# Optimization experiments

Hardware: AMD Instinct MI355X
Metric: run time of the kernel (lower is better)

Reference implementation:

```python
import jax, jax.numpy as jnp
import numpy as np

HIDDEN = 2048
NUM_HEADS = 16
HEAD_DIM = HIDDEN // NUM_HEADS  # 128
ROPE_THETA = 10000.0
T = 4096


def _rope(x, positions):
    # x: [T, H, D]; neox-style rotary (rotate halves), matching vLLM get_rope default
    half = HEAD_DIM // 2
    inv_freq = 1.0 / (ROPE_THETA ** (jnp.arange(0, half, dtype=jnp.float32) / half))
    freqs = positions.astype(jnp.float32)[:, None] * inv_freq[None, :]  # [T, half]
    cos = jnp.cos(freqs)[:, None, :]  # [T, 1, half]
    sin = jnp.sin(freqs)[:, None, :]
    x1, x2 = x[..., :half], x[..., half:]
    return jnp.concatenate([x1 * cos - x2 * sin, x2 * cos + x1 * sin], axis=-1)


def setup_inputs() -> dict:
    key = jax.random.key(0)
    k1, k2, k3 = jax.random.split(key, 3)
    return {
        "hidden_states": jax.random.normal(k1, (T, HIDDEN), dtype=jnp.float32),
        "positions": jnp.arange(T, dtype=jnp.int32),
        "w_qkv": jax.random.normal(k2, (HIDDEN, 3 * HIDDEN), dtype=jnp.float32) * (HIDDEN ** -0.5),
        "w_o": jax.random.normal(k3, (HIDDEN, HIDDEN), dtype=jnp.float32) * (HIDDEN ** -0.5),
    }


def reference(hidden_states, positions, w_qkv, w_o):
    qkv = hidden_states @ w_qkv  # [T, 3H]
    q, k, v = jnp.split(qkv, 3, axis=-1)
    q = q.reshape(T, NUM_HEADS, HEAD_DIM)
    k = k.reshape(T, NUM_HEADS, HEAD_DIM)
    v = v.reshape(T, NUM_HEADS, HEAD_DIM)
    q = _rope(q, positions)
    k = _rope(k, positions)
    scale = HEAD_DIM ** -0.5
    # causal SDPA over flattened single sequence
    scores = jnp.einsum("qhd,khd->hqk", q, k) * scale  # [H, T, T]
    causal = jnp.tril(jnp.ones((T, T), dtype=bool))
    scores = jnp.where(causal[None, :, :], scores, jnp.finfo(scores.dtype).min)
    probs = jax.nn.softmax(scores, axis=-1)
    attn = jnp.einsum("hqk,khd->qhd", probs, v).reshape(T, HIDDEN)
    return attn @ w_o
```

## Files before the change

kernel.cpp:

```cpp
#include <hip/hip_runtime.h>
#include <hip/hip_bf16.h>
#include <cstdint>
#include <cstddef>

#define T_SEQ 4096
#define HID   2048
#define NH    16
#define HD    128
#define QKVN  6144
#define KVB   32
#define CHT   16
#define CPH   144
#define SCL2  0.12753224f

typedef unsigned short u16;
typedef unsigned int u32;
typedef __bf16 bf16x8 __attribute__((ext_vector_type(8)));
typedef __bf16 bf16x4 __attribute__((ext_vector_type(4)));
typedef float  f32x4  __attribute__((ext_vector_type(4)));

typedef const __attribute__((address_space(1))) void* gas_ptr;
typedef __attribute__((address_space(3))) void* las_ptr;

__device__ __forceinline__ void async16(const void* g, void* l) {
  __builtin_amdgcn_global_load_lds((gas_ptr)g, (las_ptr)l, 16, 0, 0);
}

__device__ __forceinline__ u16 f2bf(float f) {
  unsigned int u = __float_as_uint(f);
  u += 0x7fffu + ((u >> 16) & 1u);
  return (u16)(u >> 16);
}

__device__ __forceinline__ float bf2f(u16 x) {
  return __uint_as_float((unsigned)x << 16);
}

__global__ void cast_f32_bf16(const float* __restrict__ in, u16* __restrict__ out, int n) {
  int i = (blockIdx.x * blockDim.x + threadIdx.x) * 4;
  if (i >= n) return;
  float4 v = *(const float4*)&in[i];
  uint2 o;
  o.x = (unsigned)f2bf(v.x) | ((unsigned)f2bf(v.y) << 16);
  o.y = (unsigned)f2bf(v.z) | ((unsigned)f2bf(v.w) << 16);
  *(uint2*)&out[i] = o;
}

__global__ void transpose_cast(const float* __restrict__ in, u16* __restrict__ out,
                               int R, int C) {
  __shared__ float tile[64][65];
  int c0 = blockIdx.x * 64, r0 = blockIdx.y * 64;
  int tid = threadIdx.x;
#pragma unroll
  for (int i = 0; i < 16; ++i) {
    int e = i * 256 + tid;
    int rr = e >> 6, cc = e & 63;
    tile[rr][cc] = in[(size_t)(r0 + rr) * C + c0 + cc];
  }
  __syncthreads();
#pragma unroll
  for (int i = 0; i < 16; ++i) {
    int e = i * 256 + tid;
    int oc = e >> 6, orr = e & 63;
    out[(size_t)(c0 + oc) * R + r0 + orr] = f2bf(tile[orr][oc]);
  }
}

__global__ void cs_init(const int* __restrict__ pos, float2* __restrict__ cs) {
  int idx = blockIdx.x * 256 + threadIdx.x;
  int t = idx >> 6, dt = idx & 63;
  float inv = exp2f((float)dt * -0.20762050594046932f);
  float f = (float)pos[t] * inv;
  float s, c;
  __sincosf(f, &s, &c);
  cs[idx] = make_float2(c, s);
}

template <int MODE, typename OUT>
__global__ __launch_bounds__(256)
void gemm_bf16_bt(const u16* __restrict__ A, const u16* __restrict__ BT,
                  OUT* __restrict__ C, u16* __restrict__ Qh, u16* __restrict__ Kh,
                  const float2* __restrict__ cs, int M, int N, int K) {
  __shared__ u16 As[2][128 * 32];
  __shared__ u16 Bs[2][128 * 32];
  int tid = threadIdx.x;
  int row0 = blockIdx.y * 128, col0 = blockIdx.x * 128;
  int wv = tid >> 6, lane = tid & 63, lr = lane & 15, lq = lane >> 4;
  int wm = wv * 32;
  f32x4 acc[2][8] = {};

  auto stage = [&](int buf, int ks) {
#pragma unroll
    for (int k = 0; k < 2; ++k) {
      int c = k * 256 + tid;
      int row = c >> 2, col = c & 3;
      int key = (row >> 1) & 3;
      async16(&A[(size_t)(row0 + row) * K + ks + (col ^ key) * 8], &As[buf][c * 8]);
      async16(&BT[(size_t)(col0 + row) * K + ks + (col ^ key) * 8], &Bs[buf][c * 8]);
    }
  };

  stage(0, 0);
  __syncthreads();
  int nk = K >> 5;
  for (int t = 0; t < nk; ++t) {
    int cur = t & 1;
    if (t + 1 < nk) stage(cur ^ 1, (t + 1) * 32);

    const char* AsB = (const char*)&As[cur][0];
    const char* BsB = (const char*)&Bs[cur][0];
    bf16x8 a[2], b[8];
#pragma unroll
    for (int mi = 0; mi < 2; ++mi) {
      int row = wm + mi * 16 + lr;
      a[mi] = *(const bf16x8*)(AsB + row * 64 + ((lq ^ ((row >> 1) & 3)) << 4));
    }
#pragma unroll
    for (int ni = 0; ni < 8; ++ni) {
      int row = ni * 16 + lr;
      b[ni] = *(const bf16x8*)(BsB + row * 64 + ((lq ^ ((row >> 1) & 3)) << 4));
    }
#pragma unroll
    for (int mi = 0; mi < 2; ++mi)
#pragma unroll
      for (int ni = 0; ni < 8; ++ni)
        acc[mi][ni] = __builtin_amdgcn_mfma_f32_16x16x32_bf16(a[mi], b[ni], acc[mi][ni], 0, 0, 0);
    __syncthreads();
  }

  if constexpr (MODE == 1) {
    int sec = col0 >> 11;
    int hh = (col0 & (HID - 1)) >> 7;
    if (sec < 2) {
      u16* dst = (sec == 0) ? Qh : Kh;
      float scl = (sec == 0) ? SCL2 : 1.0f;
#pragma unroll
      for (int mi = 0; mi < 2; ++mi)
#pragma unroll
        for (int r = 0; r < 4; ++r) {
          int t = row0 + wm + mi * 16 + lq * 4 + r;
#pragma unroll
          for (int nj = 0; nj < 4; ++nj) {
            float2 csv = cs[t * 64 + nj * 16 + lr];
            float v1 = acc[mi][nj][r], v2 = acc[mi][nj + 4][r];
            float o1 = (v1 * csv.x - v2 * csv.y) * scl;
            float o2 = (v2 * csv.x + v1 * csv.y) * scl;
            size_t ob = ((size_t)hh * T_SEQ + t) * HD + nj * 16 + lr;
            dst[ob] = f2bf(o1);
            dst[ob + 64] = f2bf(o2);
          }
        }
    } else {
#pragma unroll
      for (int mi = 0; mi < 2; ++mi)
#pragma unroll
        for (int ni = 0; ni < 8; ++ni)
#pragma unroll
          for (int r = 0; r < 4; ++r)
            C[(size_t)(row0 + wm + mi * 16 + lq * 4 + r) * N + col0 + ni * 16 + lr] =
                (OUT)f2bf(acc[mi][ni][r]);
    }
  } else {
#pragma unroll
    for (int mi = 0; mi < 2; ++mi)
#pragma unroll
      for (int ni = 0; ni < 8; ++ni)
#pragma unroll
        for (int r = 0; r < 4; ++r)
          C[(size_t)(row0 + wm + mi * 16 + lq * 4 + r) * N + col0 + ni * 16 + lr] =
              (OUT)acc[mi][ni][r];
  }
}

__global__ void vtrans(const u16* __restrict__ qkv, u16* __restrict__ Vt) {
  __shared__ u16 tile[64][136];
  int t0 = blockIdx.x * 64;
  int h = blockIdx.y;
  int tid = threadIdx.x;
#pragma unroll
  for (int i = 0; i < 32; ++i) {
    int e = i * 256 + tid;
    int tt = e >> 7, d = e & 127;
    tile[tt][d] = qkv[(size_t)(t0 + tt) * QKVN + 2 * HID + h * HD + d];
  }
  __syncthreads();
#pragma unroll
  for (int i = 0; i < 32; ++i) {
    int e = i * 256 + tid;
    int d = e >> 6, tt = e & 63;
    Vt[((size_t)h * HD + d) * T_SEQ + t0 + tt] = tile[tt][d];
  }
}

__global__ __launch_bounds__(256)
void attn_fwd(const u16* __restrict__ Qh, const u16* __restrict__ Kh,
              const u16* __restrict__ Vt, u16* __restrict__ Opart,
              float2* __restrict__ ml, u16* __restrict__ attn) {
  __shared__ u16 Ks[2][32 * 128];
  __shared__ u16 Vs[2][128 * 32];
  __shared__ u16 Ps[4][32 * 32];

  int tid = threadIdx.x;
  int wv = tid >> 6, lane = tid & 63, lr = lane & 15, lq = lane >> 4;
  char* PsB = (char*)&Ps[wv][0];

  int id = blockIdx.x;
  int h = id / CPH;
  int w = (CPH - 1) - (id - h * CPH);
  int slot = h * CPH + w;
  int bq = 0, acc = 0;
  for (;;) {
    int ch = (bq + 4) >> 2;
    if (w < acc + ch) break;
    acc += ch;
    ++bq;
  }
  int c = w - acc;
  int nt = 4 * bq + 4;
  int j0 = c * CHT, j1 = min(j0 + CHT, nt);
  int q0 = bq * 128, wrow0 = q0 + wv * 32;

  bf16x8 qf[2][4];
#pragma unroll
  for (int qi = 0; qi < 2; ++qi)
#pragma unroll
    for (int kd = 0; kd < 4; ++kd)
      qf[qi][kd] = *(const bf16x8*)
          &Qh[((size_t)h * T_SEQ + wrow0 + qi * 16 + lr) * HD + kd * 32 + lq * 8];

  f32x4 acc_ot[8][2] = {};
  float m_run[2] = {-1e30f, -1e30f};
  float l_run[2] = {0.0f, 0.0f};

  auto stage = [&](int buf, int jb) {
#pragma unroll
    for (int k = 0; k < 2; ++k) {
      int cc = k * 256 + tid;
      int row = cc >> 4;
      int sc = (cc ^ (row & 7)) & 15;
      async16(&Kh[((size_t)h * T_SEQ + jb + row) * HD + sc * 8], &Ks[buf][cc * 8]);
    }
#pragma unroll
    for (int k = 0; k < 2; ++k) {
      int cc = k * 256 + tid;
      int row = cc >> 2, col = cc & 3;
      int key = (row >> 1) & 3;
      async16(&Vt[((size_t)h * HD + row) * T_SEQ + jb + (col ^ key) * 8],
              &Vs[buf][cc * 8]);
    }
  };

  stage(0, j0 * KVB);
  __syncthreads();

  for (int j = j0; j < j1; ++j) {
    int cur = (j - j0) & 1;
    int jb = j * KVB;
    if (j + 1 < j1) stage(cur ^ 1, jb + KVB);

    if (jb <= wrow0 + 31) {
      const char* KsB = (const char*)&Ks[cur][0];
      const char* VsB = (const char*)&Vs[cur][0];

      f32x4 st[2][2] = {};
#pragma unroll
      for (int kd = 0; kd < 4; ++kd) {
#pragma unroll
        for (int kj = 0; kj < 2; ++kj) {
          int row = kj * 16 + lr;
          int byt = (row << 8) + kd * 64 + lq * 16;
          bf16x8 kf = *(const bf16x8*)(KsB + (byt ^ ((row & 7) << 4)));
#pragma unroll
          for (int qi = 0; qi < 2; ++qi)
            st[kj][qi] = __builtin_amdgcn_mfma_f32_16x16x32_bf16(
                kf, qf[qi][kd], st[kj][qi], 0, 0, 0);
        }
      }

      if (jb + KVB - 1 > wrow0) {
#pragma unroll
        for (int qi = 0; qi < 2; ++qi) {
          int qg = wrow0 + qi * 16 + lr;
#pragma unroll
          for (int kj = 0; kj < 2; ++kj)
#pragma unroll
            for (int r = 0; r < 4; ++r)
              if (jb + kj * 16 + lq * 4 + r > qg) st[kj][qi][r] = -1e30f;
        }
      }

      float sf[2];
#pragma unroll
      for (int qi = 0; qi < 2; ++qi) {
        float mx = fmaxf(fmaxf(fmaxf(st[0][qi][0], st[0][qi][1]),
                               fmaxf(st[0][qi][2], st[0][qi][3])),
                         fmaxf(fmaxf(st[1][qi][0], st[1][qi][1]),
                               fmaxf(st[1][qi][2], st[1][qi][3])));
        mx = fmaxf(mx, __shfl_xor(mx, 16));
        mx = fmaxf(mx, __shfl_xor(mx, 32));
        float mnew = fmaxf(m_run[qi], mx);
        sf[qi] = exp2f(m_run[qi] - mnew);
        m_run[qi] = mnew;

        int rowb = (qi * 16 + lr) * 64;
        int key = ((lr >> 1) & 3) << 4;
        float rs = 0.0f;
#pragma unroll
        for (int kj = 0; kj < 2; ++kj) {
          float p0 = exp2f(st[kj][qi][0] - mnew);
          float p1 = exp2f(st[kj][qi][1] - mnew);
          float p2 = exp2f(st[kj][qi][2] - mnew);
          float p3 = exp2f(st[kj][qi][3] - mnew);
          rs += (p0 + p1) + (p2 + p3);
          bf16x4 pk;
          pk[0] = (__bf16)p0; pk[1] = (__bf16)p1;
          pk[2] = (__bf16)p2; pk[3] = (__bf16)p3;
          *(bf16x4*)(PsB + rowb + (((kj * 16 + lq * 4) * 2) ^ key)) = pk;
        }
        l_run[qi] = l_run[qi] * sf[qi] + rs;
      }

      if (__any((sf[0] < 1.0f) || (sf[1] < 1.0f))) {
#pragma unroll
        for (int di = 0; di < 8; ++di)
#pragma unroll
          for (int qi = 0; qi < 2; ++qi)
#pragma unroll
            for (int r = 0; r < 4; ++r) acc_ot[di][qi][r] *= sf[qi];
      }

      bf16x8 pa[2];
#pragma unroll
      for (int qi = 0; qi < 2; ++qi) {
        int prow = qi * 16 + lr;
        pa[qi] = *(const bf16x8*)(PsB + prow * 64 + ((lq ^ ((lr >> 1) & 3)) << 4));
      }
#pragma unroll
      for (int di = 0; di < 8; ++di) {
        int vrow = di * 16 + lr;
        bf16x8 vb = *(const bf16x8*)(VsB + vrow * 64 + ((lq ^ ((vrow >> 1) & 3)) << 4));
#pragma unroll
        for (int qi = 0; qi < 2; ++qi)
          acc_ot[di][qi] = __builtin_amdgcn_mfma_f32_16x16x32_bf16(
              vb, pa[qi], acc_ot[di][qi], 0, 0, 0);
      }
    }
    __syncthreads();
  }

  if (bq < 4) {
#pragma unroll
    for (int qi = 0; qi < 2; ++qi) {
      float l = l_run[qi];
      l += __shfl_xor(l, 16);
      l += __shfl_xor(l, 32);
      float rl = 1.0f / l;
      int qrow = q0 + wv * 32 + qi * 16 + lr;
#pragma unroll
      for (int di = 0; di < 8; ++di) {
        bf16x4 pk;
        pk[0] = (__bf16)(acc_ot[di][qi][0] * rl);
        pk[1] = (__bf16)(acc_ot[di][qi][1] * rl);
        pk[2] = (__bf16)(acc_ot[di][qi][2] * rl);
        pk[3] = (__bf16)(acc_ot[di][qi][3] * rl);
        *(bf16x4*)&attn[(size_t)qrow * HID + h * HD + di * 16 + lq * 4] = pk;
      }
    }
  } else {
    u16* Op = Opart + (size_t)slot * 128 * 128;
#pragma unroll
    for (int qi = 0; qi < 2; ++qi) {
      float l = l_run[qi];
      l += __shfl_xor(l, 16);
      l += __shfl_xor(l, 32);
      int q = wv * 32 + qi * 16 + lr;
      if (lq == 0) ml[(size_t)slot * 128 + q] = make_float2(m_run[qi], l);
#pragma unroll
      for (int di = 0; di < 8; ++di) {
        bf16x4 pk;
        pk[0] = (__bf16)acc_ot[di][qi][0];
        pk[1] = (__bf16)acc_ot[di][qi][1];
        pk[2] = (__bf16)acc_ot[di][qi][2];
        pk[3] = (__bf16)acc_ot[di][qi][3];
        *(bf16x4*)&Op[q * 128 + di * 16 + lq * 4] = pk;
      }
    }
  }
}

__global__ __launch_bounds__(256)
void attn_combine(const u16* __restrict__ Opart, const float2* __restrict__ ml,
                  u16* __restrict__ attn) {
  int idx = blockIdx.x * 256 + threadIdx.x;
  int e8 = idx * 8;
  int qrow = e8 >> 11;
  int bq = qrow >> 7;
  if (bq < 4) return;
  int col = e8 & (HID - 1);
  int h = col >> 7, coll = col & 127;
  int ql = qrow & 127;
  int a = bq >> 2, r = bq & 3;
  int base = h * CPH + (a + 1) * (2 * a + r);
  int n = (bq + 4) >> 2;

  float m = -1e30f;
  for (int c = 0; c < n; ++c) m = fmaxf(m, ml[(size_t)(base + c) * 128 + ql].x);
  float lsum = 0.0f;
  float o[8] = {};
  for (int c = 0; c < n; ++c) {
    float2 mlc = ml[(size_t)(base + c) * 128 + ql];
    float wgt = exp2f(mlc.x - m);
    lsum += mlc.y * wgt;
    const u16* src = Opart + ((size_t)(base + c) * 128 + ql) * 128 + coll;
    ushort4 v0 = *(const ushort4*)src;
    ushort4 v1 = *(const ushort4*)(src + 4);
    o[0] += bf2f(v0.x) * wgt; o[1] += bf2f(v0.y) * wgt;
    o[2] += bf2f(v0.z) * wgt; o[3] += bf2f(v0.w) * wgt;
    o[4] += bf2f(v1.x) * wgt; o[5] += bf2f(v1.y) * wgt;
    o[6] += bf2f(v1.z) * wgt; o[7] += bf2f(v1.w) * wgt;
  }
  float rl = 1.0f / lsum;
  uint4 w;
  w.x = (u32)f2bf(o[0] * rl) | ((u32)f2bf(o[1] * rl) << 16);
  w.y = (u32)f2bf(o[2] * rl) | ((u32)f2bf(o[3] * rl) << 16);
  w.z = (u32)f2bf(o[4] * rl) | ((u32)f2bf(o[5] * rl) << 16);
  w.w = (u32)f2bf(o[6] * rl) | ((u32)f2bf(o[7] * rl) << 16);
  *(uint4*)&attn[e8] = w;
}

extern "C" void kernel_launch(void* const* d_in, const int* in_sizes, int n_in,
                              void* d_out, int out_size, void* d_ws, size_t ws_size,
                              hipStream_t stream) {
  const float* hidden    = (const float*)d_in[0];
  const int*   positions = (const int*)d_in[1];
  const float* w_qkv     = (const float*)d_in[2];
  const float* w_o       = (const float*)d_in[3];
  float* out = (float*)d_out;

  char* p = (char*)d_ws;
  u16* woT    = (u16*)p;  p += (size_t)HID * HID * 2;
  u16* Qh     = (u16*)p;  p += (size_t)T_SEQ * HID * 2;
  u16* Kh     = (u16*)p;  p += (size_t)T_SEQ * HID * 2;
  u16* Vt     = (u16*)p;  p += (size_t)T_SEQ * HID * 2;
  u16* attn_b = (u16*)p;  p += (size_t)T_SEQ * HID * 2;
  float2* cs  = (float2*)p; p += (size_t)T_SEQ * 64 * sizeof(float2);
  char* un = p;
  u16* hs_b   = (u16*)un;
  u16* wqkvT  = (u16*)(un + (size_t)T_SEQ * HID * 2);
  u16* qkvb   = (u16*)(un + (size_t)T_SEQ * HID * 2 + (size_t)QKVN * HID * 2);
  u16* Opart  = (u16*)un;
  float2* ml  = (float2*)(un + (size_t)NH * CPH * 128 * 128 * 2);

  cast_f32_bf16<<<(T_SEQ * HID / 4 + 255) / 256, 256, 0, stream>>>(hidden, hs_b, T_SEQ * HID);
  transpose_cast<<<dim3(QKVN / 64, HID / 64), 256, 0, stream>>>(w_qkv, wqkvT, HID, QKVN);
  transpose_cast<<<dim3(HID / 64, HID / 64), 256, 0, stream>>>(w_o, woT, HID, HID);
  cs_init<<<T_SEQ * 64 / 256, 256, 0, stream>>>(positions, cs);
  gemm_bf16_bt<1, u16><<<dim3(QKVN / 128, T_SEQ / 128), 256, 0, stream>>>(
      hs_b, wqkvT, qkvb, Qh, Kh, cs, T_SEQ, QKVN, HID);
  vtrans<<<dim3(T_SEQ / 64, NH), 256, 0, stream>>>(qkvb, Vt);
  attn_fwd<<<NH * CPH, 256, 0, stream>>>(Qh, Kh, Vt, Opart, ml, attn_b);
  attn_combine<<<T_SEQ * HID / 8 / 256, 256, 0, stream>>>(Opart, ml, attn_b);
  gemm_bf16_bt<0, float><<<dim3(HID / 128, T_SEQ / 128), 256, 0, stream>>>(
      attn_b, woT, out, nullptr, nullptr, nullptr, T_SEQ, HID, HID);
}
```

Before: 405.5 us.

## Fuse V transpose into new 128x256 QKV GEMM and retile output GEMM

Replaces the generic QKV GEMM with a 512-thread kernel using 128x256 tiles, a deeper K-step (64) with split async staging, explicit vmcnt waits and MFMA priority hints. It writes V directly in transposed layout via an LDS swizzled staging pass, which removes the intermediate qkv buffer and the separate vtrans kernel. The output GEMM switches to a 2x2 warp layout with 64x64 per-wave tiles for better operand reuse. The new kernel uses more LDS (96KB) and registers, and its occupancy depends on the launch bound of 2 blocks per CU.

```diff
diff --git a/kernel.cpp b/kernel.cpp
--- a/kernel.cpp
+++ b/kernel.cpp
@@ -76,18 +76,141 @@
   cs[idx] = make_float2(c, s);
 }
 
-template <int MODE, typename OUT>
+#define ABASE(b,u) (((b)*2+(u))*4096)
+#define BBASE(b,u) (16384 + ((b)*2+(u))*8192)
+
+__global__ __launch_bounds__(512, 2)
+void qkv_gemm_dp(const u16* __restrict__ A, const u16* __restrict__ BT,
+                 u16* __restrict__ Qh, u16* __restrict__ Kh, u16* __restrict__ Vt,
+                 const float2* __restrict__ cs) {
+  __shared__ __align__(16) u16 sm[49152];
+  const int K = HID;
+  int tid = threadIdx.x;
+  int wv = tid >> 6, lane = tid & 63, lr = lane & 15, lq = lane >> 4;
+  int wm = wv >> 1, wn = wv & 1;
+  int row0 = blockIdx.y * 128, col0 = blockIdx.x * 256;
+
+  auto stage_unit = [&](int b, int kt, int u) {
+    {
+      int c = tid;
+      int row = c >> 2, cg = c & 3, key = (row >> 1) & 3;
+      async16(&A[(size_t)(row0 + row) * K + kt * 64 + u * 32 + (cg ^ key) * 8],
+              &sm[ABASE(b, u) + c * 8]);
+    }
+#pragma unroll
+    for (int i = 0; i < 2; ++i) {
+      int c2 = i * 512 + tid;
+      int row = c2 >> 2, cg = c2 & 3, key = (row >> 1) & 3;
+      async16(&BT[(size_t)(col0 + row) * K + kt * 64 + u * 32 + (cg ^ key) * 8],
+              &sm[BBASE(b, u) + c2 * 8]);
+    }
+  };
+
+  f32x4 acc[2][8] = {};
+  stage_unit(0, 0, 0);
+  stage_unit(0, 0, 1);
+
+  const int nk = K / 64;
+  for (int kt = 0; kt < nk; ++kt) {
+    int b = kt & 1;
+#pragma unroll
+    for (int u = 0; u < 2; ++u) {
+      if (kt + 1 < nk) {
+        stage_unit(b ^ 1, kt + 1, u);
+        asm volatile("s_waitcnt vmcnt(6)" ::: "memory");
+      } else if (u == 0) {
+        asm volatile("s_waitcnt vmcnt(3)" ::: "memory");
+      } else {
+        asm volatile("s_waitcnt vmcnt(0)" ::: "memory");
+      }
+      __builtin_amdgcn_s_barrier();
+
+      const char* Ab = (const char*)sm + ABASE(b, u) * 2;
+      const char* Bb = (const char*)sm + BBASE(b, u) * 2;
+      bf16x8 a0, a1, bf[8];
+      {
+        int rowa = wm * 32 + lr;
+        a0 = *(const bf16x8*)(Ab + rowa * 64 + ((lq ^ ((rowa >> 1) & 3)) << 4));
+        int rowa1 = rowa + 16;
+        a1 = *(const bf16x8*)(Ab + rowa1 * 64 + ((lq ^ ((rowa1 >> 1) & 3)) << 4));
+      }
+#pragma unroll
+      for (int nj = 0; nj < 8; ++nj) {
+        int rowb = wn * 128 + nj * 16 + lr;
+        bf[nj] = *(const bf16x8*)(Bb + rowb * 64 + ((lq ^ ((rowb >> 1) & 3)) << 4));
+      }
+      __builtin_amdgcn_s_setprio(1);
+#pragma unroll
+      for (int nj = 0; nj < 8; ++nj)
+        acc[0][nj] = __builtin_amdgcn_mfma_f32_16x16x32_bf16(a0, bf[nj], acc[0][nj], 0, 0, 0);
+#pragma unroll
+      for (int nj = 0; nj < 8; ++nj)
+        acc[1][nj] = __builtin_amdgcn_mfma_f32_16x16x32_bf16(a1, bf[nj], acc[1][nj], 0, 0, 0);
+      __builtin_amdgcn_s_setprio(0);
+      __builtin_amdgcn_s_barrier();
+    }
+  }
+
+  int sec = col0 >> 11;
+  int base_h = (col0 & (HID - 1)) >> 7;
+  if (sec < 2) {
+    u16* dst = (sec == 0) ? Qh : Kh;
+    float scl = (sec == 0) ? SCL2 : 1.0f;
+    int hh = base_h + wn;
+#pragma unroll
+    for (int mi = 0; mi < 2; ++mi)
+#pragma unroll
+      for (int r = 0; r < 4; ++r) {
+        int t = row0 + wm * 32 + mi * 16 + lq * 4 + r;
+#pragma unroll
+        for (int nj = 0; nj < 4; ++nj) {
+          float2 csv = cs[t * 64 + nj * 16 + lr];
+          float v1 = acc[mi][nj][r], v2 = acc[mi][nj + 4][r];
+          size_t ob = ((size_t)hh * T_SEQ + t) * HD + nj * 16 + lr;
+          dst[ob]      = f2bf((v1 * csv.x - v2 * csv.y) * scl);
+          dst[ob + 64] = f2bf((v2 * csv.x + v1 * csv.y) * scl);
+        }
+      }
+  } else {
+    char* smB = (char*)sm;
+    __syncthreads();
+#pragma unroll
+    for (int mi = 0; mi < 2; ++mi)
+#pragma unroll
+      for (int nj = 0; nj < 8; ++nj) {
+        int d = nj * 16 + lr;
+        int tl = wm * 32 + mi * 16 + lq * 4;
+        bf16x4 pk;
+        pk[0] = (__bf16)acc[mi][nj][0];
+        pk[1] = (__bf16)acc[mi][nj][1];
+        pk[2] = (__bf16)acc[mi][nj][2];
+        pk[3] = (__bf16)acc[mi][nj][3];
+        *(bf16x4*)(smB + wn * 32768 + ((d * 256 + tl * 2) ^ ((d & 7) << 4))) = pk;
+      }
+    __syncthreads();
+#pragma unroll
+    for (int j = 0; j < 8; ++j) {
+      int g = j * 512 + tid;
+      int head = g >> 11;
+      int w2 = g & 2047;
+      int d = w2 >> 4, tc = w2 & 15;
+      bf16x8 v = *(const bf16x8*)(smB + head * 32768 +
+                                  ((d * 256 + tc * 16) ^ ((d & 7) << 4)));
+      *(bf16x8*)&Vt[((size_t)(base_h + head) * HD + d) * T_SEQ + row0 + tc * 8] = v;
+    }
+  }
+}
+
 __global__ __launch_bounds__(256)
-void gemm_bf16_bt(const u16* __restrict__ A, const u16* __restrict__ BT,
-                  OUT* __restrict__ C, u16* __restrict__ Qh, u16* __restrict__ Kh,
-                  const float2* __restrict__ cs, int M, int N, int K) {
+void gemm_out(const u16* __restrict__ A, const u16* __restrict__ BT,
+              float* __restrict__ C, int M, int N, int K) {
   __shared__ u16 As[2][128 * 32];
   __shared__ u16 Bs[2][128 * 32];
   int tid = threadIdx.x;
   int row0 = blockIdx.y * 128, col0 = blockIdx.x * 128;
   int wv = tid >> 6, lane = tid & 63, lr = lane & 15, lq = lane >> 4;
-  int wm = wv * 32;
-  f32x4 acc[2][8] = {};
+  int wm = (wv >> 1) * 64, wn = (wv & 1) * 64;
+  f32x4 acc[4][4] = {};
 
   auto stage = [&](int buf, int ks) {
 #pragma unroll
@@ -109,87 +232,33 @@
 
     const char* AsB = (const char*)&As[cur][0];
     const char* BsB = (const char*)&Bs[cur][0];
-    bf16x8 a[2], b[8];
-#pragma unroll
-    for (int mi = 0; mi < 2; ++mi) {
+    bf16x8 a[4], b[4];
+#pragma unroll
+    for (int mi = 0; mi < 4; ++mi) {
       int row = wm + mi * 16 + lr;
       a[mi] = *(const bf16x8*)(AsB + row * 64 + ((lq ^ ((row >> 1) & 3)) << 4));
     }
 #pragma unroll
-    for (int ni = 0; ni < 8; ++ni) {
-      int row = ni * 16 + lr;
+    for (int ni = 0; ni < 4; ++ni) {
+      int row = wn + ni * 16 + lr;
       b[ni] = *(const bf16x8*)(BsB + row * 64 + ((lq ^ ((row >> 1) & 3)) << 4));
     }
 #pragma unroll
-    for (int mi = 0; mi < 2; ++mi)
-#pragma unroll
-      for (int ni = 0; ni < 8; ++ni)
+    for (int mi = 0; mi < 4; ++mi)
+#pragma unroll
+      for (int ni = 0; ni < 4; ++ni)
         acc[mi][ni] = __builtin_amdgcn_mfma_f32_16x16x32_bf16(a[mi], b[ni], acc[mi][ni], 0, 0, 0);
     __syncthreads();
   }
 
-  if constexpr (MODE == 1) {
-    int sec = col0 >> 11;
-    int hh = (col0 & (HID - 1)) >> 7;
-    if (sec < 2) {
-      u16* dst = (sec == 0) ? Qh : Kh;
-      float scl = (sec == 0) ? SCL2 : 1.0f;
-#pragma unroll
-      for (int mi = 0; mi < 2; ++mi)
-#pragma unroll
-        for (int r = 0; r < 4; ++r) {
-          int t = row0 + wm + mi * 16 + lq * 4 + r;
-#pragma unroll
-          for (int nj = 0; nj < 4; ++nj) {
-            float2 csv = cs[t * 64 + nj * 16 + lr];
-            float v1 = acc[mi][nj][r], v2 = acc[mi][nj + 4][r];
-            float o1 = (v1 * csv.x - v2 * csv.y) * scl;
-            float o2 = (v2 * csv.x + v1 * csv.y) * scl;
-            size_t ob = ((size_t)hh * T_SEQ + t) * HD + nj * 16 + lr;
-            dst[ob] = f2bf(o1);
-            dst[ob + 64] = f2bf(o2);
-          }
-        }
-    } else {
-#pragma unroll
-      for (int mi = 0; mi < 2; ++mi)
-#pragma unroll
-        for (int ni = 0; ni < 8; ++ni)
-#pragma unroll
-          for (int r = 0; r < 4; ++r)
-            C[(size_t)(row0 + wm + mi * 16 + lq * 4 + r) * N + col0 + ni * 16 + lr] =
-                (OUT)f2bf(acc[mi][ni][r]);
-    }
-  } else {
-#pragma unroll
-    for (int mi = 0; mi < 2; ++mi)
-#pragma unroll
-      for (int ni = 0; ni < 8; ++ni)
-#pragma unroll
-        for (int r = 0; r < 4; ++r)
-          C[(size_t)(row0 + wm + mi * 16 + lq * 4 + r) * N + col0 + ni * 16 + lr] =
-              (OUT)acc[mi][ni][r];
-  }
-}
-
-__global__ void vtrans(const u16* __restrict__ qkv, u16* __restrict__ Vt) {
-  __shared__ u16 tile[64][136];
-  int t0 = blockIdx.x * 64;
-  int h = blockIdx.y;
-  int tid = threadIdx.x;
-#pragma unroll
-  for (int i = 0; i < 32; ++i) {
-    int e = i * 256 + tid;
-    int tt = e >> 7, d = e & 127;
-    tile[tt][d] = qkv[(size_t)(t0 + tt) * QKVN + 2 * HID + h * HD + d];
-  }
-  __syncthreads();
-#pragma unroll
-  for (int i = 0; i < 32; ++i) {
-    int e = i * 256 + tid;
-    int d = e >> 6, tt = e & 63;
-    Vt[((size_t)h * HD + d) * T_SEQ + t0 + tt] = tile[tt][d];
-  }
+#pragma unroll
+  for (int mi = 0; mi < 4; ++mi)
+#pragma unroll
+    for (int ni = 0; ni < 4; ++ni)
+#pragma unroll
+      for (int r = 0; r < 4; ++r)
+        C[(size_t)(row0 + wm + mi * 16 + lq * 4 + r) * N + col0 + wn + ni * 16 + lr] =
+            acc[mi][ni][r];
 }
 
 __global__ __launch_bounds__(256)
@@ -447,7 +516,6 @@
   char* un = p;
   u16* hs_b   = (u16*)un;
   u16* wqkvT  = (u16*)(un + (size_t)T_SEQ * HID * 2);
-  u16* qkvb   = (u16*)(un + (size_t)T_SEQ * HID * 2 + (size_t)QKVN * HID * 2);
   u16* Opart  = (u16*)un;
   float2* ml  = (float2*)(un + (size_t)NH * CPH * 128 * 128 * 2);
 
@@ -455,11 +523,10 @@
   transpose_cast<<<dim3(QKVN / 64, HID / 64), 256, 0, stream>>>(w_qkv, wqkvT, HID, QKVN);
   transpose_cast<<<dim3(HID / 64, HID / 64), 256, 0, stream>>>(w_o, woT, HID, HID);
   cs_init<<<T_SEQ * 64 / 256, 256, 0, stream>>>(positions, cs);
-  gemm_bf16_bt<1, u16><<<dim3(QKVN / 128, T_SEQ / 128), 256, 0, stream>>>(
-      hs_b, wqkvT, qkvb, Qh, Kh, cs, T_SEQ, QKVN, HID);
-  vtrans<<<dim3(T_SEQ / 64, NH), 256, 0, stream>>>(qkvb, Vt);
+  qkv_gemm_dp<<<dim3(QKVN / 256, T_SEQ / 128), 512, 0, stream>>>(
+      hs_b, wqkvT, Qh, Kh, Vt, cs);
   attn_fwd<<<NH * CPH, 256, 0, stream>>>(Qh, Kh, Vt, Opart, ml, attn_b);
   attn_combine<<<T_SEQ * HID / 8 / 256, 256, 0, stream>>>(Opart, ml, attn_b);
-  gemm_bf16_bt<0, float><<<dim3(HID / 128, T_SEQ / 128), 256, 0, stream>>>(
-      attn_b, woT, out, nullptr, nullptr, nullptr, T_SEQ, HID, HID);
-}
+  gemm_out<<<dim3(HID / 128, T_SEQ / 128), 256, 0, stream>>>(attn_b, woT, out,
+                                                             T_SEQ, HID, HID);
+}
```

Result: faster. 389.2 us (-4.0%).
